# Optimization experiments

Hardware: AMD Instinct MI355X
Metric: run time of the kernel (lower is better)

The kernel has to match this reference:

```python
import jax, jax.numpy as jnp
import numpy as np

DILS = [2 ** i for i in range(9)] * 7  # 27 residual-only layers + 36 layers with skip
N0 = 27  # first 27 layers (dilations0) do not contribute to skip connections


def _dconv(x, w, b, d):
    # dilated 'same' conv1d: x [B,C,T], w [O,I,3]
    y = jax.lax.conv_general_dilated(x, w, (1,), [(d, d)], rhs_dilation=(d,),
                                     dimension_numbers=('NCH', 'OIH', 'NCH'))
    return y + b[None, :, None]


def _pw(x, w, b):
    # 1x1 conv: w [O,C], x [B,C,T]
    return jnp.einsum('oc,bct->bot', w, x) + b[None, :, None]


def setup_inputs() -> dict:
    key = jax.random.key(0)
    ks = jax.random.split(key, 13)
    B, T, rd, sd, qd, L = 8, 16384, 128, 128, 256, 63
    s = 0.05
    f = lambda k, sh: jax.random.normal(k, sh, jnp.float32) * s
    return {
        'x': jax.random.normal(ks[0], (B, 1, T), jnp.float32),
        'causal_w': f(ks[1], (rd, 1, 25)),
        'causal_b': f(ks[2], (rd,)),
        'dcnn_w': f(ks[3], (L, rd, rd, 3)),
        'dcnn_b': f(ks[4], (L, rd)),
        'dense_w': f(ks[5], (L, rd, rd)),
        'dense_b': f(ks[6], (L, rd)),
        'skip_w': f(ks[7], (L, sd, rd)),
        'skip_b': f(ks[8], (L, sd)),
        'post1_w': f(ks[9], (sd, sd)),
        'post1_b': f(ks[10], (sd,)),
        'post2_w': f(ks[11], (qd, sd)),
        'post2_b': f(ks[12], (qd,)),
    }


def reference(x, causal_w, causal_b, dcnn_w, dcnn_b, dense_w, dense_b,
              skip_w, skip_b, post1_w, post1_b, post2_w, post2_b):
    # causal conv: kernel 25, padding 12 ('same')
    x = jax.lax.conv_general_dilated(x, causal_w, (1,), [(12, 12)],
                                     dimension_numbers=('NCH', 'OIH', 'NCH'))
    x = x + causal_b[None, :, None]
    B, _, T = x.shape
    skip = jnp.zeros((B, skip_w.shape[1], T), x.dtype)
    for cnt, d in enumerate(DILS):
        xin = x
        h = jax.nn.relu(x)
        h = jax.nn.relu(_dconv(h, dcnn_w[cnt], dcnn_b[cnt], d))
        if cnt >= N0:
            skip = skip + _pw(h, skip_w[cnt], skip_b[cnt])
        x = _pw(h, dense_w[cnt], dense_b[cnt]) + xin
    h = jax.nn.relu(_pw(jax.nn.relu(skip), post1_w, post1_b))
    return _pw(h, post2_w, post2_b)
```

## Files before the change

### kernel.cpp

```cpp
#include <hip/hip_runtime.h>

#define RD     128
#define TT     128
#define TLEN   16384
#define NB     8
#define NLAYER 63
#define N0SKIP 27
#define NSKIP  36
#define QD     256
#define PADR   136
#define CROWS  256

typedef short bf16x8 __attribute__((ext_vector_type(8)));
typedef float f32x4  __attribute__((ext_vector_type(4)));

__device__ __forceinline__ unsigned short f2bf(float f) {
  unsigned u = __float_as_uint(f);
  u += 0x7fffu + ((u >> 16) & 1u);
  return (unsigned short)(u >> 16);
}
__device__ __forceinline__ unsigned short f2bf_relu(float f) {
  f = f > 0.f ? f : 0.f;
  unsigned u = __float_as_uint(f);
  u += 0x7fffu + ((u >> 16) & 1u);
  return (unsigned short)(u >> 16);
}

__device__ __forceinline__ void zero_acc(f32x4 (&acc)[4][4]) {
#pragma unroll
  for (int i = 0; i < 4; ++i)
#pragma unroll
    for (int j = 0; j < 4; ++j) acc[i][j] = (f32x4){0.f, 0.f, 0.f, 0.f};
}

template <bool ACT_A>
__device__ __forceinline__ void gemm128(const unsigned short* __restrict__ w,
                                        const short* sx, const int rows[4],
                                        int c0w, int n, int q, f32x4 (&acc)[4][4]) {
#pragma unroll
  for (int ks = 0; ks < 4; ++ks) {
    const int i0 = ks * 32 + q * 8;
    bf16x8 wf[4], af[4];
#pragma unroll
    for (int ct = 0; ct < 4; ++ct)
      wf[ct] = *(const bf16x8*)&w[(size_t)(c0w + ct * 16 + n) * RD + i0];
#pragma unroll
    for (int tt = 0; tt < 4; ++tt)
      af[tt] = *(const bf16x8*)&sx[rows[tt] * PADR + i0];
#pragma unroll
    for (int ct = 0; ct < 4; ++ct)
#pragma unroll
      for (int tt = 0; tt < 4; ++tt)
        acc[ct][tt] = ACT_A
          ? __builtin_amdgcn_mfma_f32_16x16x32_bf16(af[tt], wf[ct], acc[ct][tt], 0, 0, 0)
          : __builtin_amdgcn_mfma_f32_16x16x32_bf16(wf[ct], af[tt], acc[ct][tt], 0, 0, 0);
  }
}

__device__ __forceinline__ void stage_xr(short* sx, const unsigned short* __restrict__ xg,
                                         int tstart, int nrows, int slot0, int tid) {
  const int tot = nrows << 4;
  for (int idx = tid; idx < tot; idx += 256) {
    const int r = idx >> 4, ck = (idx & 15) << 3;
    const int tg = tstart + r;
    uint4 v = {0u, 0u, 0u, 0u};
    if ((unsigned)tg < (unsigned)TLEN) v = *(const uint4*)&xg[(size_t)tg * RD + ck];
    *(uint4*)&sx[(slot0 + r) * PADR + ck] = v;
  }
}

__device__ __forceinline__ void stage_tile(short* dst, const unsigned short* __restrict__ src,
                                           int tid) {
  for (int idx = tid; idx < 128 * 16; idx += 256) {
    const int r = idx >> 4, ck = (idx & 15) << 3;
    *(uint4*)&dst[r * PADR + ck] = *(const uint4*)&src[(size_t)r * RD + ck];
  }
}

__device__ __forceinline__ void store_act(short* sx, const f32x4 (&acc)[4][4],
                                          const float* __restrict__ bias,
                                          int c0w, int t0w, int n, int q) {
#pragma unroll
  for (int ct = 0; ct < 4; ++ct) {
    const int c = c0w + ct * 16 + n;
    const float bb = bias[c];
#pragma unroll
    for (int tt = 0; tt < 4; ++tt) {
      const int tb = t0w + tt * 16 + q * 4;
#pragma unroll
      for (int r = 0; r < 4; ++r)
        sx[(tb + r) * PADR + c] = (short)f2bf_relu(acc[ct][tt][r] + bb);
    }
  }
}

__global__ __launch_bounds__(256, 2) void layer_kernel(
    const unsigned short* __restrict__ xr_in, const float* __restrict__ x_in,
    float* __restrict__ x_out, unsigned short* __restrict__ xr_out,
    unsigned short* __restrict__ h_out,
    float* __restrict__ skip,
    const unsigned short* __restrict__ wconv, const float* __restrict__ bconv,
    const unsigned short* __restrict__ wdense, const float* __restrict__ bdense,
    const unsigned short* __restrict__ wskip, const float* __restrict__ bskip,
    int dil) {
  __shared__ short sx[CROWS * PADR];

  const int tid = threadIdx.x;
  const int b   = blockIdx.x >> 7;
  const int t0  = (blockIdx.x & 127) << 7;
  const int lane = tid & 63;
  const int n = lane & 15, q = lane >> 4;
  const int wv = tid >> 6;
  const int c0w = (wv & 1) * 64, t0w = (wv >> 1) * 64;
  const unsigned short* xrb = xr_in + (size_t)b * TLEN * RD;

  f32x4 acc[4][4];
  zero_acc(acc);
  int rows[4];

  if (dil <= 64) {
    stage_xr(sx, xrb, t0 - dil, 128 + 2 * dil, 0, tid);
    __syncthreads();
#pragma unroll
    for (int k = 0; k < 3; ++k) {
#pragma unroll
      for (int tt = 0; tt < 4; ++tt) rows[tt] = t0w + tt * 16 + n + k * dil;
      gemm128<true>(wconv + (size_t)k * RD * RD, sx, rows, c0w, n, q, acc);
    }
  } else {
    stage_xr(sx, xrb, t0 - dil, 128, 0, tid);
    __syncthreads();
    stage_xr(sx, xrb, t0, 128, 128, tid);
#pragma unroll
    for (int tt = 0; tt < 4; ++tt) rows[tt] = t0w + tt * 16 + n;
    gemm128<true>(wconv, sx, rows, c0w, n, q, acc);
    __syncthreads();
    stage_xr(sx, xrb, t0 + dil, 128, 0, tid);
#pragma unroll
    for (int tt = 0; tt < 4; ++tt) rows[tt] = 128 + t0w + tt * 16 + n;
    gemm128<true>(wconv + (size_t)RD * RD, sx, rows, c0w, n, q, acc);
    __syncthreads();
#pragma unroll
    for (int tt = 0; tt < 4; ++tt) rows[tt] = t0w + tt * 16 + n;
    gemm128<true>(wconv + (size_t)2 * RD * RD, sx, rows, c0w, n, q, acc);
  }
  __syncthreads();

  store_act(sx, acc, bconv, c0w, t0w, n, q);
  __syncthreads();

  if (h_out) {
    unsigned short* hb = h_out + ((size_t)b * TLEN + t0) * RD;
    for (int idx = tid; idx < 128 * 16; idx += 256) {
      const int r = idx >> 4, ck = (idx & 15) << 3;
      *(uint4*)&hb[(size_t)r * RD + ck] = *(const uint4*)&sx[r * PADR + ck];
    }
  }

  zero_acc(acc);
#pragma unroll
  for (int tt = 0; tt < 4; ++tt) rows[tt] = t0w + tt * 16 + n;
  gemm128<true>(wdense, sx, rows, c0w, n, q, acc);
  {
    const size_t tb_g = ((size_t)b * TLEN + t0) * RD;
    const float* xi = x_in + tb_g;
    float* xo = x_out + tb_g;
    unsigned short* xro = xr_out + tb_g;
#pragma unroll
    for (int ct = 0; ct < 4; ++ct) {
      const int c = c0w + ct * 16 + n;
      const float bd = bdense[c];
#pragma unroll
      for (int tt = 0; tt < 4; ++tt) {
        const int tb = t0w + tt * 16 + q * 4;
#pragma unroll
        for (int r = 0; r < 4; ++r) {
          const int t = tb + r;
          const float v = xi[(size_t)t * RD + c] + acc[ct][tt][r] + bd;
          xo[(size_t)t * RD + c] = v;
          xro[(size_t)t * RD + c] = f2bf_relu(v);
        }
      }
    }
  }

  if (skip) {
    zero_acc(acc);
    gemm128<true>(wskip, sx, rows, c0w, n, q, acc);
    float* sp = skip + ((size_t)b * TLEN + t0) * RD;
#pragma unroll
    for (int ct = 0; ct < 4; ++ct) {
      const int c = c0w + ct * 16 + n;
      const float bs = bskip[c];
#pragma unroll
      for (int tt = 0; tt < 4; ++tt) {
        const int tb = t0w + tt * 16 + q * 4;
#pragma unroll
        for (int r = 0; r < 4; ++r) {
          const int t = tb + r;
          sp[(size_t)t * RD + c] += acc[ct][tt][r] + bs;
        }
      }
    }
  }
}

__global__ __launch_bounds__(256, 2) void gather_kernel(
    const unsigned short* __restrict__ h, int nl,
    const unsigned short* __restrict__ wsk_g,
    float* __restrict__ skip_io, int skip_rd, int do_final,
    const float* __restrict__ bsum,
    const unsigned short* __restrict__ p1, const float* __restrict__ p1b,
    const unsigned short* __restrict__ p2, const float* __restrict__ p2b,
    float* __restrict__ out) {
  __shared__ short buf[2][128 * PADR];

  const int tid = threadIdx.x;
  const int b   = blockIdx.x >> 7;
  const int t0  = (blockIdx.x & 127) << 7;
  const int lane = tid & 63;
  const int n = lane & 15, q = lane >> 4;
  const int wv = tid >> 6;
  const int c0w = (wv & 1) * 64, t0w = (wv >> 1) * 64;
  const size_t tilebase = ((size_t)b * TLEN + t0) * RD;
  const size_t XNE = (size_t)NB * TLEN * RD;

  f32x4 acc[4][4];
  zero_acc(acc);
  int rows[4];
#pragma unroll
  for (int tt = 0; tt < 4; ++tt) rows[tt] = t0w + tt * 16 + n;

  if (nl > 0) {
    stage_tile(buf[0], h + tilebase, tid);
    __syncthreads();
    for (int li = 0; li < nl; ++li) {
      const int cur = li & 1;
      if (li + 1 < nl)
        stage_tile(buf[cur ^ 1], h + (size_t)(li + 1) * XNE + tilebase, tid);
      gemm128<true>(wsk_g + (size_t)li * RD * RD, buf[cur], rows, c0w, n, q, acc);
      __syncthreads();
    }
  }

  if (!do_final) {
    float* sp = skip_io + tilebase;
#pragma unroll
    for (int ct = 0; ct < 4; ++ct) {
      const int c = c0w + ct * 16 + n;
#pragma unroll
      for (int tt = 0; tt < 4; ++tt) {
        const int tb = t0w + tt * 16 + q * 4;
#pragma unroll
        for (int r = 0; r < 4; ++r) {
          float v = acc[ct][tt][r];
          if (skip_rd) v += sp[(size_t)(tb + r) * RD + c];
          sp[(size_t)(tb + r) * RD + c] = v;
        }
      }
    }
    return;
  }

  if (skip_rd) {
    const float* sp = skip_io + tilebase;
#pragma unroll
    for (int ct = 0; ct < 4; ++ct) {
      const int c = c0w + ct * 16 + n;
#pragma unroll
      for (int tt = 0; tt < 4; ++tt) {
        const int tb = t0w + tt * 16 + q * 4;
#pragma unroll
        for (int r = 0; r < 4; ++r)
          acc[ct][tt][r] += sp[(size_t)(tb + r) * RD + c];
      }
    }
  }

  store_act(buf[0], acc, bsum, c0w, t0w, n, q);
  __syncthreads();
  zero_acc(acc);
  gemm128<true>(p1, buf[0], rows, c0w, n, q, acc);
  store_act(buf[1], acc, p1b, c0w, t0w, n, q);
  __syncthreads();

  for (int half = 0; half < 2; ++half) {
    zero_acc(acc);
    gemm128<false>(p2 + (size_t)half * RD * RD, buf[1], rows, c0w, n, q, acc);
    const size_t obase = ((size_t)b * QD + half * RD) * TLEN + t0;
#pragma unroll
    for (int ct = 0; ct < 4; ++ct) {
      const int cb = c0w + ct * 16 + q * 4;
      const float4 bb = *(const float4*)&p2b[half * RD + cb];
      const float bv[4] = {bb.x, bb.y, bb.z, bb.w};
#pragma unroll
      for (int tt = 0; tt < 4; ++tt) {
        const int t = t0w + tt * 16 + n;
#pragma unroll
        for (int r = 0; r < 4; ++r)
          out[obase + (size_t)(cb + r) * TLEN + t] = acc[ct][tt][r] + bv[r];
      }
    }
  }
}

__global__ __launch_bounds__(256) void causal_kernel(const float* __restrict__ x,
                                                     const float* __restrict__ w,
                                                     const float* __restrict__ bias,
                                                     float* __restrict__ y,
                                                     unsigned short* __restrict__ yr) {
  __shared__ float xw[152];
  __shared__ float wl[RD * 25];
  __shared__ float bl[RD];
  const int tid = threadIdx.x;
  const int b   = blockIdx.x >> 7;
  const int t0  = (blockIdx.x & 127) << 7;
  for (int i = tid; i < RD * 25; i += 256) wl[i] = w[i];
  if (tid < RD) bl[tid] = bias[tid];
  for (int i = tid; i < 152; i += 256) {
    const int tg = t0 - 12 + i;
    xw[i] = ((unsigned)tg < (unsigned)TLEN) ? x[(size_t)b * TLEN + tg] : 0.f;
  }
  __syncthreads();
  const int c = tid & 127, tp = tid >> 7;
  float* yb = y + ((size_t)b * TLEN + t0) * RD + c;
  unsigned short* yrb = yr + ((size_t)b * TLEN + t0) * RD + c;
  const float bc = bl[c];
  for (int i = 0; i < 64; ++i) {
    const int tl = i * 2 + tp;
    float s = bc;
#pragma unroll
    for (int k = 0; k < 25; ++k) s = fmaf(wl[c * 25 + k], xw[tl + k], s);
    yb[(size_t)tl * RD] = s;
    yrb[(size_t)tl * RD] = f2bf_relu(s);
  }
}

__global__ __launch_bounds__(256) void cvt_kernel(const float* __restrict__ in,
                                                  unsigned short* __restrict__ out,
                                                  int total) {
  const int i = blockIdx.x * 256 + threadIdx.x;
  if (i < total) out[i] = f2bf(in[i]);
}
__global__ __launch_bounds__(256) void cvt_conv_kernel(const float* __restrict__ in,
                                                       unsigned short* __restrict__ out,
                                                       int total) {
  const int idx = blockIdx.x * 256 + threadIdx.x;
  if (idx >= total) return;
  const int ci = idx & 127, co = (idx >> 7) & 127, lk = idx >> 14;
  const int k = lk % 3, l = lk / 3;
  out[idx] = f2bf(in[(((size_t)l * RD + co) * RD + ci) * 3 + k]);
}
__global__ void bsum_kernel(const float* __restrict__ sb, float* __restrict__ bsum) {
  const int c = threadIdx.x;
  float s = 0.f;
  for (int l = N0SKIP; l < NLAYER; ++l) s += sb[l * RD + c];
  bsum[c] = s;
}

extern "C" void kernel_launch(void* const* d_in, const int* in_sizes, int n_in,
                              void* d_out, int out_size, void* d_ws, size_t ws_size,
                              hipStream_t stream) {
  const float* x        = (const float*)d_in[0];
  const float* causal_w = (const float*)d_in[1];
  const float* causal_b = (const float*)d_in[2];
  const float* dcnn_w   = (const float*)d_in[3];
  const float* dcnn_b   = (const float*)d_in[4];
  const float* dense_w  = (const float*)d_in[5];
  const float* dense_b  = (const float*)d_in[6];
  const float* skip_w   = (const float*)d_in[7];
  const float* skip_b   = (const float*)d_in[8];
  const float* post1_w  = (const float*)d_in[9];
  const float* post1_b  = (const float*)d_in[10];
  const float* post2_w  = (const float*)d_in[11];
  const float* post2_b  = (const float*)d_in[12];
  float* out = (float*)d_out;

  const size_t XNE = (size_t)NB * TLEN * RD;

  char* p = (char*)d_ws;
  float* bsm = (float*)p;                    p += 512;
  unsigned short* wc  = (unsigned short*)p;  p += (size_t)NLAYER * 3 * RD * RD * 2;
  unsigned short* wd  = (unsigned short*)p;  p += (size_t)NLAYER * RD * RD * 2;
  unsigned short* wsk = (unsigned short*)p;  p += (size_t)NLAYER * RD * RD * 2;
  unsigned short* p1  = (unsigned short*)p;  p += RD * RD * 2;
  unsigned short* p2  = (unsigned short*)p;  p += QD * RD * 2;
  float* xA           = (float*)p;           p += XNE * 4;
  float* xB           = (float*)p;           p += XNE * 4;
  unsigned short* xrA = (unsigned short*)p;  p += XNE * 2;
  unsigned short* xrB = (unsigned short*)p;  p += XNE * 2;
  const size_t base_used = (size_t)(p - (char*)d_ws);

  const size_t need_full = base_used + (size_t)NSKIP * XNE * 2;
  const size_t need_g9   = base_used + XNE * 4 + (size_t)9 * XNE * 2;
  int G;
  if (ws_size >= need_full)    G = NSKIP;
  else if (ws_size >= need_g9) G = 9;
  else                         G = 0;

  float* skp = nullptr;
  unsigned short* hb = nullptr;
  if (G == NSKIP) {
    hb = (unsigned short*)p;
  } else {
    skp = (float*)p; p += XNE * 4;
    if (G == 9) hb = (unsigned short*)p;
  }

  const int tconv = NLAYER * 3 * RD * RD;
  const int t2    = NLAYER * RD * RD;
  cvt_conv_kernel<<<(tconv + 255) / 256, 256, 0, stream>>>(dcnn_w, wc, tconv);
  cvt_kernel<<<(t2 + 255) / 256, 256, 0, stream>>>(dense_w, wd, t2);
  cvt_kernel<<<(t2 + 255) / 256, 256, 0, stream>>>(skip_w, wsk, t2);
  cvt_kernel<<<(RD * RD + 255) / 256, 256, 0, stream>>>(post1_w, p1, RD * RD);
  cvt_kernel<<<(QD * RD + 255) / 256, 256, 0, stream>>>(post2_w, p2, QD * RD);
  if (G > 0) bsum_kernel<<<1, RD, 0, stream>>>(skip_b, bsm);
  else       hipMemsetAsync(bsm, 0, 512, stream);
  if (G == 0) hipMemsetAsync(skp, 0, XNE * 4, stream);

  const int grid = NB * (TLEN / TT);
  causal_kernel<<<grid, 256, 0, stream>>>(x, causal_w, causal_b, xA, xrA);

  const float* xs = xA;  float* xd = xB;
  const unsigned short* xrs = xrA;  unsigned short* xrd = xrB;

  for (int l = 0; l < NLAYER; ++l) {
    const int dil = 1 << (l % 9);
    unsigned short* hout = nullptr;
    float* skarg = nullptr;
    if (l >= N0SKIP) {
      if (G > 0) hout = hb + (size_t)((l - N0SKIP) % G) * XNE;
      else       skarg = skp;
    }
    layer_kernel<<<grid, 256, 0, stream>>>(
        xrs, xs, xd, xrd, hout, skarg,
        wc  + (size_t)l * 3 * RD * RD, dcnn_b  + (size_t)l * RD,
        wd  + (size_t)l * RD * RD,     dense_b + (size_t)l * RD,
        wsk + (size_t)l * RD * RD,     skip_b  + (size_t)l * RD,
        dil);
    { const float* t = xs; xs = xd; xd = (float*)t; }
    { const unsigned short* t = xrs; xrs = xrd; xrd = (unsigned short*)t; }

    if (G == 9 && l >= N0SKIP && ((l - N0SKIP) % 9) == 8) {
      const int g  = (l - N0SKIP) / 9;
      const int l0 = N0SKIP + g * 9;
      const int fg = (g == 3);
      gather_kernel<<<grid, 256, 0, stream>>>(
          hb, 9, wsk + (size_t)l0 * RD * RD,
          skp, (g > 0) ? 1 : 0, fg,
          bsm, p1, post1_b, p2, post2_b, out);
    }
  }

  if (G == NSKIP) {
    gather_kernel<<<grid, 256, 0, stream>>>(
        hb, NSKIP, wsk + (size_t)N0SKIP * RD * RD,
        nullptr, 0, 1, bsm, p1, post1_b, p2, post2_b, out);
  } else if (G == 0) {
    gather_kernel<<<grid, 256, 0, stream>>>(
        nullptr, 0, nullptr, skp, 1, 1, bsm, p1, post1_b, p2, post2_b, out);
  }
}
```

Before: 6.029 ms.

## Store residual as bf16 hi/lo pair, shrink LDS, raise occupancy

Replaces the fp32 residual plus separate relu-bf16 copy with a split bf16 hi/lo pair, so relu is applied on the fly while staging the hi half into LDS. This is meant to cut per-layer global traffic. LDS rows drop from 256 to 192 so three blocks fit per CU, and the dil=64 path now uses one staged window plus a ring-wrapped refill. The skip accumulator becomes bf16 and gather batching adapts to the available workspace, which risks precision loss in the skip sum.

```diff
diff --git a/kernel.cpp b/kernel.cpp
--- a/kernel.cpp
+++ b/kernel.cpp
@@ -9,7 +9,7 @@
 #define NSKIP  36
 #define QD     256
 #define PADR   136
-#define CROWS  256
+#define CROWS  192
 
 typedef short bf16x8 __attribute__((ext_vector_type(8)));
 typedef float f32x4  __attribute__((ext_vector_type(4)));
@@ -25,6 +25,13 @@
   u += 0x7fffu + ((u >> 16) & 1u);
   return (unsigned short)(u >> 16);
 }
+__device__ __forceinline__ float bf2f(unsigned short s) {
+  return __uint_as_float(((unsigned)s) << 16);
+}
+__device__ __forceinline__ unsigned relu2(unsigned v) {
+  unsigned m = (v & 0x80008000u) >> 15;
+  return v & ~((m << 16) - m);
+}
 
 __device__ __forceinline__ void zero_acc(f32x4 (&acc)[4][4]) {
 #pragma unroll
@@ -57,7 +64,7 @@
   }
 }
 
-__device__ __forceinline__ void stage_xr(short* sx, const unsigned short* __restrict__ xg,
+__device__ __forceinline__ void stage_hi(short* sx, const unsigned short* __restrict__ xg,
                                          int tstart, int nrows, int slot0, int tid) {
   const int tot = nrows << 4;
   for (int idx = tid; idx < tot; idx += 256) {
@@ -65,6 +72,7 @@
     const int tg = tstart + r;
     uint4 v = {0u, 0u, 0u, 0u};
     if ((unsigned)tg < (unsigned)TLEN) v = *(const uint4*)&xg[(size_t)tg * RD + ck];
+    v.x = relu2(v.x); v.y = relu2(v.y); v.z = relu2(v.z); v.w = relu2(v.w);
     *(uint4*)&sx[(slot0 + r) * PADR + ck] = v;
   }
 }
@@ -94,11 +102,11 @@
   }
 }
 
-__global__ __launch_bounds__(256, 2) void layer_kernel(
-    const unsigned short* __restrict__ xr_in, const float* __restrict__ x_in,
-    float* __restrict__ x_out, unsigned short* __restrict__ xr_out,
+__global__ __launch_bounds__(256, 3) void layer_kernel(
+    const unsigned short* __restrict__ hi_in, const unsigned short* __restrict__ lo_in,
+    unsigned short* __restrict__ hi_out, unsigned short* __restrict__ lo_out,
     unsigned short* __restrict__ h_out,
-    float* __restrict__ skip,
+    unsigned short* __restrict__ skipacc,
     const unsigned short* __restrict__ wconv, const float* __restrict__ bconv,
     const unsigned short* __restrict__ wdense, const float* __restrict__ bdense,
     const unsigned short* __restrict__ wskip, const float* __restrict__ bskip,
@@ -112,14 +120,14 @@
   const int n = lane & 15, q = lane >> 4;
   const int wv = tid >> 6;
   const int c0w = (wv & 1) * 64, t0w = (wv >> 1) * 64;
-  const unsigned short* xrb = xr_in + (size_t)b * TLEN * RD;
+  const unsigned short* hib = hi_in + (size_t)b * TLEN * RD;
 
   f32x4 acc[4][4];
   zero_acc(acc);
   int rows[4];
 
-  if (dil <= 64) {
-    stage_xr(sx, xrb, t0 - dil, 128 + 2 * dil, 0, tid);
+  if (dil <= 32) {
+    stage_hi(sx, hib, t0 - dil, 128 + 2 * dil, 0, tid);
     __syncthreads();
 #pragma unroll
     for (int k = 0; k < 3; ++k) {
@@ -127,22 +135,34 @@
       for (int tt = 0; tt < 4; ++tt) rows[tt] = t0w + tt * 16 + n + k * dil;
       gemm128<true>(wconv + (size_t)k * RD * RD, sx, rows, c0w, n, q, acc);
     }
-  } else {
-    stage_xr(sx, xrb, t0 - dil, 128, 0, tid);
+  } else if (dil == 64) {
+    stage_hi(sx, hib, t0 - 64, 192, 0, tid);
     __syncthreads();
-    stage_xr(sx, xrb, t0, 128, 128, tid);
 #pragma unroll
     for (int tt = 0; tt < 4; ++tt) rows[tt] = t0w + tt * 16 + n;
     gemm128<true>(wconv, sx, rows, c0w, n, q, acc);
-    __syncthreads();
-    stage_xr(sx, xrb, t0 + dil, 128, 0, tid);
-#pragma unroll
-    for (int tt = 0; tt < 4; ++tt) rows[tt] = 128 + t0w + tt * 16 + n;
+#pragma unroll
+    for (int tt = 0; tt < 4; ++tt) rows[tt] = t0w + tt * 16 + n + 64;
     gemm128<true>(wconv + (size_t)RD * RD, sx, rows, c0w, n, q, acc);
     __syncthreads();
+    stage_hi(sx, hib, t0 + 128, 64, 0, tid);
+    __syncthreads();
+#pragma unroll
+    for (int tt = 0; tt < 4; ++tt) {
+      int r = t0w + tt * 16 + n + 128;
+      if (r >= CROWS) r -= CROWS;
+      rows[tt] = r;
+    }
+    gemm128<true>(wconv + (size_t)2 * RD * RD, sx, rows, c0w, n, q, acc);
+  } else {
 #pragma unroll
     for (int tt = 0; tt < 4; ++tt) rows[tt] = t0w + tt * 16 + n;
-    gemm128<true>(wconv + (size_t)2 * RD * RD, sx, rows, c0w, n, q, acc);
+    for (int k = 0; k < 3; ++k) {
+      if (k) __syncthreads();
+      stage_hi(sx, hib, t0 + (k - 1) * dil, 128, 0, tid);
+      __syncthreads();
+      gemm128<true>(wconv + (size_t)k * RD * RD, sx, rows, c0w, n, q, acc);
+    }
   }
   __syncthreads();
 
@@ -163,9 +183,10 @@
   gemm128<true>(wdense, sx, rows, c0w, n, q, acc);
   {
     const size_t tb_g = ((size_t)b * TLEN + t0) * RD;
-    const float* xi = x_in + tb_g;
-    float* xo = x_out + tb_g;
-    unsigned short* xro = xr_out + tb_g;
+    const unsigned short* hi_i = hi_in + tb_g;
+    const unsigned short* lo_i = lo_in + tb_g;
+    unsigned short* hi_o = hi_out + tb_g;
+    unsigned short* lo_o = lo_out + tb_g;
 #pragma unroll
     for (int ct = 0; ct < 4; ++ct) {
       const int c = c0w + ct * 16 + n;
@@ -175,19 +196,21 @@
         const int tb = t0w + tt * 16 + q * 4;
 #pragma unroll
         for (int r = 0; r < 4; ++r) {
-          const int t = tb + r;
-          const float v = xi[(size_t)t * RD + c] + acc[ct][tt][r] + bd;
-          xo[(size_t)t * RD + c] = v;
-          xro[(size_t)t * RD + c] = f2bf_relu(v);
+          const size_t o = (size_t)(tb + r) * RD + c;
+          const float xv = bf2f(hi_i[o]) + bf2f(lo_i[o]);
+          const float v = xv + acc[ct][tt][r] + bd;
+          const unsigned short hv = f2bf(v);
+          hi_o[o] = hv;
+          lo_o[o] = f2bf(v - bf2f(hv));
         }
       }
     }
   }
 
-  if (skip) {
+  if (skipacc) {
     zero_acc(acc);
     gemm128<true>(wskip, sx, rows, c0w, n, q, acc);
-    float* sp = skip + ((size_t)b * TLEN + t0) * RD;
+    unsigned short* sp = skipacc + ((size_t)b * TLEN + t0) * RD;
 #pragma unroll
     for (int ct = 0; ct < 4; ++ct) {
       const int c = c0w + ct * 16 + n;
@@ -197,8 +220,8 @@
         const int tb = t0w + tt * 16 + q * 4;
 #pragma unroll
         for (int r = 0; r < 4; ++r) {
-          const int t = tb + r;
-          sp[(size_t)t * RD + c] += acc[ct][tt][r] + bs;
+          const size_t o = (size_t)(tb + r) * RD + c;
+          sp[o] = f2bf(bf2f(sp[o]) + acc[ct][tt][r] + bs);
         }
       }
     }
@@ -208,7 +231,7 @@
 __global__ __launch_bounds__(256, 2) void gather_kernel(
     const unsigned short* __restrict__ h, int nl,
     const unsigned short* __restrict__ wsk_g,
-    float* __restrict__ skip_io, int skip_rd, int do_final,
+    unsigned short* __restrict__ skipacc, int skip_rd, int do_final,
     const float* __restrict__ bsum,
     const unsigned short* __restrict__ p1, const float* __restrict__ p1b,
     const unsigned short* __restrict__ p2, const float* __restrict__ p2b,
@@ -243,8 +266,8 @@
     }
   }
 
-  if (!do_final) {
-    float* sp = skip_io + tilebase;
+  if (skip_rd) {
+    const unsigned short* sp = skipacc + tilebase;
 #pragma unroll
     for (int ct = 0; ct < 4; ++ct) {
       const int c = c0w + ct * 16 + n;
@@ -252,18 +275,14 @@
       for (int tt = 0; tt < 4; ++tt) {
         const int tb = t0w + tt * 16 + q * 4;
 #pragma unroll
-        for (int r = 0; r < 4; ++r) {
-          float v = acc[ct][tt][r];
-          if (skip_rd) v += sp[(size_t)(tb + r) * RD + c];
-          sp[(size_t)(tb + r) * RD + c] = v;
-        }
-      }
-    }
-    return;
-  }
-
-  if (skip_rd) {
-    const float* sp = skip_io + tilebase;
+        for (int r = 0; r < 4; ++r)
+          acc[ct][tt][r] += bf2f(sp[(size_t)(tb + r) * RD + c]);
+      }
+    }
+  }
+
+  if (!do_final) {
+    unsigned short* sp = skipacc + tilebase;
 #pragma unroll
     for (int ct = 0; ct < 4; ++ct) {
       const int c = c0w + ct * 16 + n;
@@ -272,9 +291,10 @@
         const int tb = t0w + tt * 16 + q * 4;
 #pragma unroll
         for (int r = 0; r < 4; ++r)
-          acc[ct][tt][r] += sp[(size_t)(tb + r) * RD + c];
-      }
-    }
+          sp[(size_t)(tb + r) * RD + c] = f2bf(acc[ct][tt][r]);
+      }
+    }
+    return;
   }
 
   store_act(buf[0], acc, bsum, c0w, t0w, n, q);
@@ -307,8 +327,8 @@
 __global__ __launch_bounds__(256) void causal_kernel(const float* __restrict__ x,
                                                      const float* __restrict__ w,
                                                      const float* __restrict__ bias,
-                                                     float* __restrict__ y,
-                                                     unsigned short* __restrict__ yr) {
+                                                     unsigned short* __restrict__ hi,
+                                                     unsigned short* __restrict__ lo) {
   __shared__ float xw[152];
   __shared__ float wl[RD * 25];
   __shared__ float bl[RD];
@@ -323,16 +343,17 @@
   }
   __syncthreads();
   const int c = tid & 127, tp = tid >> 7;
-  float* yb = y + ((size_t)b * TLEN + t0) * RD + c;
-  unsigned short* yrb = yr + ((size_t)b * TLEN + t0) * RD + c;
+  unsigned short* hib = hi + ((size_t)b * TLEN + t0) * RD + c;
+  unsigned short* lob = lo + ((size_t)b * TLEN + t0) * RD + c;
   const float bc = bl[c];
   for (int i = 0; i < 64; ++i) {
     const int tl = i * 2 + tp;
     float s = bc;
 #pragma unroll
     for (int k = 0; k < 25; ++k) s = fmaf(wl[c * 25 + k], xw[tl + k], s);
-    yb[(size_t)tl * RD] = s;
-    yrb[(size_t)tl * RD] = f2bf_relu(s);
+    const unsigned short hv = f2bf(s);
+    hib[(size_t)tl * RD] = hv;
+    lob[(size_t)tl * RD] = f2bf(s - bf2f(hv));
   }
 }
 
@@ -385,26 +406,25 @@
   unsigned short* wsk = (unsigned short*)p;  p += (size_t)NLAYER * RD * RD * 2;
   unsigned short* p1  = (unsigned short*)p;  p += RD * RD * 2;
   unsigned short* p2  = (unsigned short*)p;  p += QD * RD * 2;
-  float* xA           = (float*)p;           p += XNE * 4;
-  float* xB           = (float*)p;           p += XNE * 4;
-  unsigned short* xrA = (unsigned short*)p;  p += XNE * 2;
-  unsigned short* xrB = (unsigned short*)p;  p += XNE * 2;
+  unsigned short* hiA = (unsigned short*)p;  p += XNE * 2;
+  unsigned short* hiB = (unsigned short*)p;  p += XNE * 2;
+  unsigned short* loA = (unsigned short*)p;  p += XNE * 2;
+  unsigned short* loB = (unsigned short*)p;  p += XNE * 2;
   const size_t base_used = (size_t)(p - (char*)d_ws);
 
-  const size_t need_full = base_used + (size_t)NSKIP * XNE * 2;
-  const size_t need_g9   = base_used + XNE * 4 + (size_t)9 * XNE * 2;
-  int G;
-  if (ws_size >= need_full)    G = NSKIP;
-  else if (ws_size >= need_g9) G = 9;
-  else                         G = 0;
-
-  float* skp = nullptr;
+  int G = 0;
+  unsigned short* skipacc = nullptr;
   unsigned short* hb = nullptr;
-  if (G == NSKIP) {
+  if (ws_size >= base_used + (size_t)NSKIP * XNE * 2) {
+    G = NSKIP;
     hb = (unsigned short*)p;
   } else {
-    skp = (float*)p; p += XNE * 4;
-    if (G == 9) hb = (unsigned short*)p;
+    skipacc = (unsigned short*)p; p += XNE * 2;
+    const size_t avail = (ws_size > (size_t)(p - (char*)d_ws))
+                             ? ws_size - (size_t)(p - (char*)d_ws) : 0;
+    G = (int)(avail / (XNE * 2));
+    if (G > NSKIP - 1) G = NSKIP - 1;
+    if (G > 0) hb = (unsigned short*)p;
   }
 
   const int tconv = NLAYER * 3 * RD * RD;
@@ -416,48 +436,49 @@
   cvt_kernel<<<(QD * RD + 255) / 256, 256, 0, stream>>>(post2_w, p2, QD * RD);
   if (G > 0) bsum_kernel<<<1, RD, 0, stream>>>(skip_b, bsm);
   else       hipMemsetAsync(bsm, 0, 512, stream);
-  if (G == 0) hipMemsetAsync(skp, 0, XNE * 4, stream);
+  if (G == 0) hipMemsetAsync(skipacc, 0, XNE * 2, stream);
 
   const int grid = NB * (TLEN / TT);
-  causal_kernel<<<grid, 256, 0, stream>>>(x, causal_w, causal_b, xA, xrA);
-
-  const float* xs = xA;  float* xd = xB;
-  const unsigned short* xrs = xrA;  unsigned short* xrd = xrB;
-
+  causal_kernel<<<grid, 256, 0, stream>>>(x, causal_w, causal_b, hiA, loA);
+
+  const unsigned short* his = hiA;  unsigned short* hid = hiB;
+  const unsigned short* los = loA;  unsigned short* lod = loB;
+
+  int done = 0, pending = 0;
   for (int l = 0; l < NLAYER; ++l) {
     const int dil = 1 << (l % 9);
     unsigned short* hout = nullptr;
-    float* skarg = nullptr;
+    unsigned short* skarg = nullptr;
     if (l >= N0SKIP) {
-      if (G > 0) hout = hb + (size_t)((l - N0SKIP) % G) * XNE;
-      else       skarg = skp;
+      if (G > 0) hout = hb + (size_t)pending * XNE;
+      else       skarg = skipacc;
     }
     layer_kernel<<<grid, 256, 0, stream>>>(
-        xrs, xs, xd, xrd, hout, skarg,
+        his, los, hid, lod, hout, skarg,
         wc  + (size_t)l * 3 * RD * RD, dcnn_b  + (size_t)l * RD,
         wd  + (size_t)l * RD * RD,     dense_b + (size_t)l * RD,
         wsk + (size_t)l * RD * RD,     skip_b  + (size_t)l * RD,
         dil);
-    { const float* t = xs; xs = xd; xd = (float*)t; }
-    { const unsigned short* t = xrs; xrs = xrd; xrd = (unsigned short*)t; }
-
-    if (G == 9 && l >= N0SKIP && ((l - N0SKIP) % 9) == 8) {
-      const int g  = (l - N0SKIP) / 9;
-      const int l0 = N0SKIP + g * 9;
-      const int fg = (g == 3);
-      gather_kernel<<<grid, 256, 0, stream>>>(
-          hb, 9, wsk + (size_t)l0 * RD * RD,
-          skp, (g > 0) ? 1 : 0, fg,
-          bsm, p1, post1_b, p2, post2_b, out);
-    }
-  }
-
-  if (G == NSKIP) {
+    { const unsigned short* t = his; his = hid; hid = (unsigned short*)t; }
+    { const unsigned short* t = los; los = lod; lod = (unsigned short*)t; }
+
+    if (l >= N0SKIP && G > 0) {
+      ++pending;
+      const int last = (l == NLAYER - 1);
+      if (pending == G || last) {
+        gather_kernel<<<grid, 256, 0, stream>>>(
+            hb, pending, wsk + (size_t)(N0SKIP + done) * RD * RD,
+            skipacc, (done > 0) ? 1 : 0, last,
+            bsm, p1, post1_b, p2, post2_b, out);
+        done += pending;
+        pending = 0;
+      }
+    }
+  }
+
+  if (G == 0) {
     gather_kernel<<<grid, 256, 0, stream>>>(
-        hb, NSKIP, wsk + (size_t)N0SKIP * RD * RD,
-        nullptr, 0, 1, bsm, p1, post1_b, p2, post2_b, out);
-  } else if (G == 0) {
-    gather_kernel<<<grid, 256, 0, stream>>>(
-        nullptr, 0, nullptr, skp, 1, 1, bsm, p1, post1_b, p2, post2_b, out);
-  }
-}
+        nullptr, 0, nullptr, skipacc, 1, 1,
+        bsm, p1, post1_b, p2, post2_b, out);
+  }
+}
```

Measured after the change: 6.925 ms. 1.15x slower.
